# Performance work log

Hardware: AMD Instinct MI355X
Metric: run time of the kernel (lower is better)

## Reference

```python
import jax, jax.numpy as jnp
import numpy as np

B, S, D = 16, 2048, 128  # batch*heads, seq_len, head_dim


def setup_inputs() -> dict:
    key = jax.random.key(0)
    kq, kk, kv, ks = jax.random.split(key, 4)
    q = jax.random.normal(kq, (B, S, D), dtype=jnp.float32)
    k = jax.random.normal(kk, (B, S, D), dtype=jnp.float32)
    v = jax.random.normal(kv, (B, S, D), dtype=jnp.float32)
    # full-shape scale tensor; keep values away from zero (~sqrt(D))
    inv_scale_factor = jax.random.uniform(ks, (B, S, S), dtype=jnp.float32,
                                          minval=8.0, maxval=16.0)
    return {"q": q, "k": k, "v": v,
            "inv_scale_factor": inv_scale_factor,
            "dropout_p": 0}


def reference(q, k, v, inv_scale_factor, dropout_p):
    # qk = q @ k^T  -> [B, Sq, Skv]
    qk = jnp.einsum('bqd,bkd->bqk', q, k)
    # elementwise divide by full-shape tensor (blocks fused SDPA dispatch)
    scaled_qk = qk / inv_scale_factor
    attn = jax.nn.softmax(scaled_qk, axis=-1)
    # dropout with p=0 is the identity (F.dropout scales by 1/(1-p) == 1)
    y = jnp.einsum('bqk,bkd->bqd', attn, v)
    return y
```

## Files before the change

kernel.cpp:

```cpp
#include <hip/hip_runtime.h>
#include <hip/hip_bf16.h>

#define BATCH 16
#define SEQ   2048
#define HD    128
#define QBLK  64
#define KVBLK 32
#define NT    (SEQ / KVBLK)
#define NW    4

typedef __attribute__((ext_vector_type(8))) short bf16x8;
typedef __attribute__((ext_vector_type(4))) float f32x4;
typedef __attribute__((ext_vector_type(4))) short s16x4;

__device__ __forceinline__ short f2bf(float x) {
    __hip_bfloat16 h = __float2bfloat16(x);
    return *reinterpret_cast<short*>(&h);
}

__global__ __launch_bounds__(256, 2)
void attn_fused(const float* __restrict__ Q, const float* __restrict__ K,
                const float* __restrict__ V, const float* __restrict__ ISF,
                float* __restrict__ O)
{
    const int tid  = threadIdx.x;
    const int lane = tid & 63;
    const int wv   = tid >> 6;
    const int lg   = lane >> 4;
    const int lc   = lane & 15;

    const int bidx = blockIdx.x;
    const int b    = bidx >> 5;
    const int q0   = (bidx & 31) * QBLK;
    const int tofs = (bidx & 1) * (NT / 2);

    __shared__ short Klds[2][32 * 128];
    __shared__ short Vtlds[2][128 * 40];
    __shared__ short Plds[NW * 16 * 40];

    bf16x8 qf[4];
    {
        const float* qrow = Q + ((size_t)b * SEQ + q0 + wv * 16 + lc) * HD;
        #pragma unroll
        for (int ks = 0; ks < 4; ++ks) {
            const float* p = qrow + ks * 32 + lg * 8;
            float4 x0 = *reinterpret_cast<const float4*>(p);
            float4 x1 = *reinterpret_cast<const float4*>(p + 4);
            bf16x8 f;
            f[0]=f2bf(x0.x); f[1]=f2bf(x0.y); f[2]=f2bf(x0.z); f[3]=f2bf(x0.w);
            f[4]=f2bf(x1.x); f[5]=f2bf(x1.y); f[6]=f2bf(x1.z); f[7]=f2bf(x1.w);
            qf[ks] = f;
        }
    }

    f32x4 oacc[8];
    #pragma unroll
    for (int i = 0; i < 8; ++i) oacc[i] = (f32x4){0.f, 0.f, 0.f, 0.f};
    float l_part[4] = {0.f, 0.f, 0.f, 0.f};

    const float* kbase = K + (size_t)b * SEQ * HD;
    const float* vbase = V + (size_t)b * SEQ * HD;
    const float* ibase = ISF + ((size_t)b * SEQ + q0 + wv * 16) * SEQ;

    float4 kreg[4];
    float  vreg[4][4];
    float  isf_cur[8], isf_nxt[8];

    auto LOAD = [&](int kv0) {
        const float* kb = kbase + (size_t)kv0 * HD;
        const float* vb = vbase + (size_t)kv0 * HD;
        #pragma unroll
        for (int r = 0; r < 4; ++r) {
            int idx = r * 256 + tid;
            kreg[r] = *reinterpret_cast<const float4*>(kb + (size_t)(idx >> 5) * HD + (idx & 31) * 4);
        }
        #pragma unroll
        for (int r = 0; r < 4; ++r) {
            int idx = r * 256 + tid;
            int d = idx & 127, kq = idx >> 7;
            #pragma unroll
            for (int j = 0; j < 4; ++j)
                vreg[r][j] = vb[(size_t)(kq * 4 + j) * HD + d];
        }
    };
    auto LOAD_ISF = [&](int kv0, float* dst) {
        #pragma unroll
        for (int nt = 0; nt < 2; ++nt)
            #pragma unroll
            for (int r = 0; r < 4; ++r)
                dst[nt * 4 + r] = ibase[(size_t)(lg * 4 + r) * SEQ + kv0 + nt * 16 + lc];
    };
    auto STORE = [&](int buf) {
        #pragma unroll
        for (int r = 0; r < 4; ++r) {
            int idx = r * 256 + tid;
            int kvr = idx >> 5, d4 = idx & 31;
            s16x4 s;
            s[0]=f2bf(kreg[r].x); s[1]=f2bf(kreg[r].y); s[2]=f2bf(kreg[r].z); s[3]=f2bf(kreg[r].w);
            int chunk = (d4 >> 1) ^ (kvr & 7);
            *reinterpret_cast<s16x4*>(&Klds[buf][kvr * 128 + chunk * 8 + (d4 & 1) * 4]) = s;
        }
        #pragma unroll
        for (int r = 0; r < 4; ++r) {
            int idx = r * 256 + tid;
            int d = idx & 127, kq = idx >> 7;
            s16x4 s;
            #pragma unroll
            for (int j = 0; j < 4; ++j) s[j] = f2bf(vreg[r][j]);
            *reinterpret_cast<s16x4*>(&Vtlds[buf][d * 40 + kq * 4]) = s;
        }
    };

    auto KV0 = [&](int t) { return (((t + tofs) & (NT - 1)) * KVBLK); };

    LOAD(KV0(0));
    LOAD_ISF(KV0(0), isf_nxt);
    STORE(0);
    __syncthreads();
    #pragma unroll
    for (int i = 0; i < 8; ++i)
        isf_cur[i] = __builtin_amdgcn_rcpf(isf_nxt[i]) * 1.44269504f;

    int cur = 0;
    for (int t = 0; t < NT; ++t) {
        const bool more = (t + 1 < NT);
        if (more) { LOAD(KV0(t + 1)); LOAD_ISF(KV0(t + 1), isf_nxt); }

        f32x4 sacc[2];
        sacc[0] = (f32x4){0.f,0.f,0.f,0.f};
        sacc[1] = (f32x4){0.f,0.f,0.f,0.f};
        __builtin_amdgcn_s_setprio(1);
        #pragma unroll
        for (int nt = 0; nt < 2; ++nt) {
            int n = lc + nt * 16;
            #pragma unroll
            for (int ks = 0; ks < 4; ++ks) {
                int chunk = (ks * 4 + lg) ^ (n & 7);
                bf16x8 bf = *reinterpret_cast<const bf16x8*>(&Klds[cur][n * 128 + chunk * 8]);
                sacc[nt] = __builtin_amdgcn_mfma_f32_16x16x32_bf16(qf[ks], bf, sacc[nt], 0, 0, 0);
            }
        }
        __builtin_amdgcn_s_setprio(0);

        short pb[2][4];
        #pragma unroll
        for (int nt = 0; nt < 2; ++nt)
            #pragma unroll
            for (int r = 0; r < 4; ++r) {
                float p = __builtin_amdgcn_exp2f(sacc[nt][r] * isf_cur[nt * 4 + r]);
                l_part[r] += p;
                pb[nt][r] = f2bf(p);
            }

        short* pw = &Plds[wv * 16 * 40];
        #pragma unroll
        for (int nt = 0; nt < 2; ++nt)
            #pragma unroll
            for (int r = 0; r < 4; ++r)
                pw[(lg * 4 + r) * 40 + nt * 16 + lc] = pb[nt][r];
        bf16x8 pa = *reinterpret_cast<const bf16x8*>(&pw[lc * 40 + lg * 8]);

        __builtin_amdgcn_s_setprio(1);
        #pragma unroll
        for (int dt = 0; dt < 8; ++dt) {
            bf16x8 vf = *reinterpret_cast<const bf16x8*>(&Vtlds[cur][(lc + dt * 16) * 40 + lg * 8]);
            oacc[dt] = __builtin_amdgcn_mfma_f32_16x16x32_bf16(pa, vf, oacc[dt], 0, 0, 0);
        }
        __builtin_amdgcn_s_setprio(0);

        if (more) STORE(cur ^ 1);
        __syncthreads();
        cur ^= 1;
        #pragma unroll
        for (int i = 0; i < 8; ++i)
            isf_cur[i] = __builtin_amdgcn_rcpf(isf_nxt[i]) * 1.44269504f;
    }

    #pragma unroll
    for (int msk = 1; msk < 16; msk <<= 1)
        #pragma unroll
        for (int r = 0; r < 4; ++r)
            l_part[r] += __shfl_xor(l_part[r], msk, 64);

    float* ob = O + ((size_t)b * SEQ + q0 + wv * 16) * HD;
    #pragma unroll
    for (int r = 0; r < 4; ++r) {
        float inv_l = 1.0f / l_part[r];
        float* orow = ob + (size_t)(lg * 4 + r) * HD;
        #pragma unroll
        for (int dt = 0; dt < 8; ++dt)
            orow[lc + dt * 16] = oacc[dt][r] * inv_l;
    }
}

extern "C" void kernel_launch(void* const* d_in, const int* in_sizes, int n_in,
                              void* d_out, int out_size, void* d_ws, size_t ws_size,
                              hipStream_t stream) {
    const float* q   = (const float*)d_in[0];
    const float* k   = (const float*)d_in[1];
    const float* v   = (const float*)d_in[2];
    const float* isf = (const float*)d_in[3];
    float* out = (float*)d_out;
    dim3 grid(BATCH * (SEQ / QBLK));
    attn_fused<<<grid, 256, 0, stream>>>(q, k, v, isf, out);
}
```

Before: 108.9 us.

## Software-pipeline QK and PV across iterations with triple-buffered V tiles

Restructures the KV loop so each iteration runs the QK MFMAs for tile t together with the PV MFMAs for tile t-1, letting the softmax/exp work and the P round-trip through LDS overlap with matrix work. V is now triple-buffered in LDS to hold the previous tile while the next one is being stored, and a prologue and epilogue handle the first and last tiles. This aims to shorten the serial dependency chain within each iteration, at the cost of about 10 KB more LDS and more live registers, which could reduce occupancy below 2 blocks per CU.

```diff
diff --git a/kernel.cpp b/kernel.cpp
--- a/kernel.cpp
+++ b/kernel.cpp
@@ -35,7 +35,7 @@
     const int tofs = (bidx & 1) * (NT / 2);
 
     __shared__ short Klds[2][32 * 128];
-    __shared__ short Vtlds[2][128 * 40];
+    __shared__ short Vtlds[3][128 * 40];
     __shared__ short Plds[NW * 16 * 40];
 
     bf16x8 qf[4];
@@ -90,7 +90,7 @@
             for (int r = 0; r < 4; ++r)
                 dst[nt * 4 + r] = ibase[(size_t)(lg * 4 + r) * SEQ + kv0 + nt * 16 + lc];
     };
-    auto STORE = [&](int buf) {
+    auto STOREK = [&](int buf) {
         #pragma unroll
         for (int r = 0; r < 4; ++r) {
             int idx = r * 256 + tid;
@@ -100,6 +100,8 @@
             int chunk = (d4 >> 1) ^ (kvr & 7);
             *reinterpret_cast<s16x4*>(&Klds[buf][kvr * 128 + chunk * 8 + (d4 & 1) * 4]) = s;
         }
+    };
+    auto STOREV = [&](int buf) {
         #pragma unroll
         for (int r = 0; r < 4; ++r) {
             int idx = r * 256 + tid;
@@ -110,38 +112,10 @@
             *reinterpret_cast<s16x4*>(&Vtlds[buf][d * 40 + kq * 4]) = s;
         }
     };
-
     auto KV0 = [&](int t) { return (((t + tofs) & (NT - 1)) * KVBLK); };
 
-    LOAD(KV0(0));
-    LOAD_ISF(KV0(0), isf_nxt);
-    STORE(0);
-    __syncthreads();
-    #pragma unroll
-    for (int i = 0; i < 8; ++i)
-        isf_cur[i] = __builtin_amdgcn_rcpf(isf_nxt[i]) * 1.44269504f;
-
-    int cur = 0;
-    for (int t = 0; t < NT; ++t) {
-        const bool more = (t + 1 < NT);
-        if (more) { LOAD(KV0(t + 1)); LOAD_ISF(KV0(t + 1), isf_nxt); }
-
-        f32x4 sacc[2];
-        sacc[0] = (f32x4){0.f,0.f,0.f,0.f};
-        sacc[1] = (f32x4){0.f,0.f,0.f,0.f};
-        __builtin_amdgcn_s_setprio(1);
-        #pragma unroll
-        for (int nt = 0; nt < 2; ++nt) {
-            int n = lc + nt * 16;
-            #pragma unroll
-            for (int ks = 0; ks < 4; ++ks) {
-                int chunk = (ks * 4 + lg) ^ (n & 7);
-                bf16x8 bf = *reinterpret_cast<const bf16x8*>(&Klds[cur][n * 128 + chunk * 8]);
-                sacc[nt] = __builtin_amdgcn_mfma_f32_16x16x32_bf16(qf[ks], bf, sacc[nt], 0, 0, 0);
-            }
-        }
-        __builtin_amdgcn_s_setprio(0);
-
+    short* pw = &Plds[wv * 16 * 40];
+    auto MAKE_PA = [&](const f32x4* sacc) -> bf16x8 {
         short pb[2][4];
         #pragma unroll
         for (int nt = 0; nt < 2; ++nt)
@@ -151,30 +125,91 @@
                 l_part[r] += p;
                 pb[nt][r] = f2bf(p);
             }
-
-        short* pw = &Plds[wv * 16 * 40];
         #pragma unroll
         for (int nt = 0; nt < 2; ++nt)
             #pragma unroll
             for (int r = 0; r < 4; ++r)
                 pw[(lg * 4 + r) * 40 + nt * 16 + lc] = pb[nt][r];
-        bf16x8 pa = *reinterpret_cast<const bf16x8*>(&pw[lc * 40 + lg * 8]);
-
+        return *reinterpret_cast<const bf16x8*>(&pw[lc * 40 + lg * 8]);
+    };
+    auto QK = [&](int buf, f32x4* sacc) {
+        #pragma unroll
+        for (int nt = 0; nt < 2; ++nt) {
+            int n = lc + nt * 16;
+            #pragma unroll
+            for (int ks = 0; ks < 4; ++ks) {
+                int chunk = (ks * 4 + lg) ^ (n & 7);
+                bf16x8 bf = *reinterpret_cast<const bf16x8*>(&Klds[buf][n * 128 + chunk * 8]);
+                sacc[nt] = __builtin_amdgcn_mfma_f32_16x16x32_bf16(qf[ks], bf, sacc[nt], 0, 0, 0);
+            }
+        }
+    };
+    auto PV = [&](bf16x8 pa, int vbuf) {
+        #pragma unroll
+        for (int dt = 0; dt < 8; ++dt) {
+            bf16x8 vf = *reinterpret_cast<const bf16x8*>(&Vtlds[vbuf][(lc + dt * 16) * 40 + lg * 8]);
+            oacc[dt] = __builtin_amdgcn_mfma_f32_16x16x32_bf16(pa, vf, oacc[dt], 0, 0, 0);
+        }
+    };
+
+    LOAD(KV0(0));
+    LOAD_ISF(KV0(0), isf_nxt);
+    STOREK(0);
+    STOREV(0);
+    __syncthreads();
+    #pragma unroll
+    for (int i = 0; i < 8; ++i)
+        isf_cur[i] = __builtin_amdgcn_rcpf(isf_nxt[i]) * 1.44269504f;
+
+    bf16x8 pa_prev;
+    {
+        LOAD(KV0(1));
+        LOAD_ISF(KV0(1), isf_nxt);
+        f32x4 sacc[2];
+        sacc[0] = (f32x4){0.f,0.f,0.f,0.f};
+        sacc[1] = (f32x4){0.f,0.f,0.f,0.f};
         __builtin_amdgcn_s_setprio(1);
-        #pragma unroll
-        for (int dt = 0; dt < 8; ++dt) {
-            bf16x8 vf = *reinterpret_cast<const bf16x8*>(&Vtlds[cur][(lc + dt * 16) * 40 + lg * 8]);
-            oacc[dt] = __builtin_amdgcn_mfma_f32_16x16x32_bf16(pa, vf, oacc[dt], 0, 0, 0);
-        }
+        QK(0, sacc);
         __builtin_amdgcn_s_setprio(0);
-
-        if (more) STORE(cur ^ 1);
+        pa_prev = MAKE_PA(sacc);
+        STOREK(1);
+        STOREV(1);
         __syncthreads();
-        cur ^= 1;
         #pragma unroll
         for (int i = 0; i < 8; ++i)
             isf_cur[i] = __builtin_amdgcn_rcpf(isf_nxt[i]) * 1.44269504f;
     }
+
+    int cur = 1, v_prev = 0, v_next = 2;
+    for (int t = 1; t < NT; ++t) {
+        const bool more = (t + 1 < NT);
+        if (more) { LOAD(KV0(t + 1)); LOAD_ISF(KV0(t + 1), isf_nxt); }
+
+        f32x4 sacc[2];
+        sacc[0] = (f32x4){0.f,0.f,0.f,0.f};
+        sacc[1] = (f32x4){0.f,0.f,0.f,0.f};
+        __builtin_amdgcn_s_setprio(1);
+        QK(cur, sacc);
+        PV(pa_prev, v_prev);
+        __builtin_amdgcn_s_setprio(0);
+
+        bf16x8 pa_cur = MAKE_PA(sacc);
+
+        if (more) { STOREK(cur ^ 1); STOREV(v_next); }
+        __syncthreads();
+
+        pa_prev = pa_cur;
+        cur ^= 1;
+        v_prev = (v_prev == 2) ? 0 : v_prev + 1;
+        v_next = (v_next == 2) ? 0 : v_next + 1;
+        #pragma unroll
+        for (int i = 0; i < 8; ++i)
+            isf_cur[i] = __builtin_amdgcn_rcpf(isf_nxt[i]) * 1.44269504f;
+    }
+
+    __builtin_amdgcn_s_setprio(1);
+    PV(pa_prev, v_prev);
+    __builtin_amdgcn_s_setprio(0);
 
     #pragma unroll
     for (int msk = 1; msk < 16; msk <<= 1)
```

After: 119.2 us. +9.4%, slower.
